# Performance work log

Hardware: AMD Instinct MI355X
Metric: run time of the kernel (lower is better)

## Reference

```python
import jax, jax.numpy as jnp
import numpy as np

B, T, I, H, NM = 128, 512, 2, 1024, 8
MS = H // NM  # module size = 128


def setup_inputs() -> dict:
    key = jax.random.key(0)
    ks = jax.random.split(key, 6)
    s = 1.0 / np.sqrt(H)
    return {
        "x": jax.random.normal(ks[0], (B, T + 1, I, 1), jnp.float32),
        "W_ih": jax.random.normal(ks[1], (H, I), jnp.float32) * s,
        "W_hh": jax.random.normal(ks[2], (H, H), jnp.float32) * s,
        "fc_w": jax.random.normal(ks[3], (I, H), jnp.float32) * s,
        "fc_b": jax.random.normal(ks[4], (I,), jnp.float32) * s,
        "enc_w": jax.random.normal(ks[5], (H, I), jnp.float32) * s,
    }


def reference(x, W_ih, W_hh, fc_w, fc_b, enc_w):
    # x: [B, T+1, I, 1] -> squeeze trailing dim
    xs = x[..., 0]                       # [B, T+1, I]
    h0 = xs[:, 0] @ enc_w.T              # start_encoder (no bias) -> [B, H]

    # Clockwork block structure: row-module i reads hidden cols >= i*MS.
    mod_idx = jnp.arange(H) // MS
    mask_hh = (mod_idx[None, :] >= mod_idx[:, None]).astype(W_hh.dtype)
    Whh_m = W_hh * mask_hh               # block upper-triangular recurrent weights
    periods = 2 ** jnp.arange(NM)        # module clock periods [1,2,4,...,128]

    def step(h, inp):
        x_t, t = inp                     # x_t: [B, I], t: scalar step index
        cand = jnp.tanh(x_t @ W_ih.T + h @ Whh_m.T)          # [B, H]
        active = jnp.repeat((t % periods) == 0, MS)          # [H] unit-level clock mask
        h_new = jnp.where(active[None, :], cand, h)          # inactive modules keep state
        return h_new, h_new @ fc_w.T + fc_b                  # fc output per step

    _, outs = jax.lax.scan(step, h0, (jnp.swapaxes(xs[:, 1:], 0, 1), jnp.arange(T)))
    return jnp.swapaxes(outs, 0, 1)      # [B, T, I]
```

## Files before the change

### kernel.cpp

```cpp
#include <hip/hip_runtime.h>
#include <hip/hip_fp16.h>
#include <math.h>

#define Bsz 128
#define Tsz 512
#define Hsz 1024
#define MS  128
#define NT  512


__global__ __launch_bounds__(256)
void retile_whh(const float* __restrict__ W, float* __restrict__ WB0,
                __half* __restrict__ WBr) {
    const int p = blockIdx.x;
    const int t = threadIdx.x;
    if (p == 0) {
        for (int idx = t; idx < MS*MS; idx += 256) {
            const int row = idx >> 7, j = idx & (MS-1);
            WB0[idx] = W[row * Hsz + j];
        }
        return;
    }
    int c = 0;
    while ((c+1)*(c+2)/2 <= p) ++c;
    const int r = p - c*(c+1)/2;
    __half* wb = WBr + (size_t)(p-1) * MS * MS;
    for (int idx = t; idx < MS*MS; idx += 256) {
        const int row = idx >> 7, j = idx & (MS-1);
        wb[idx] = __float2half(W[(size_t)(r*MS+row)*Hsz + c*MS + j]);
    }
}

__device__ __forceinline__ float fast_tanh(float x) {
    const float e = __expf(2.0f * x);
    return 1.0f - 2.0f * __builtin_amdgcn_rcpf(e + 1.0f);
}

template <int CTRL>
__device__ __forceinline__ float dpp_get(float v) {
    union { float f; int i; } u, o;
    u.f = v;
    o.i = __builtin_amdgcn_update_dpp(0, u.i, CTRL, 0xf, 0xf, true);
    return o.f;
}

union H4 { short4 s4; __half2 h2[2]; };

__global__ __launch_bounds__(NT)
void cwrnn_kernel(const float* __restrict__ x,
                  const float* __restrict__ W_ih,
                  const float* __restrict__ fc_w,
                  const float* __restrict__ fc_b,
                  const float* __restrict__ enc_w,
                  const float* __restrict__ WB0,
                  const __half* __restrict__ WBr,
                  float* __restrict__ out)
{
    __shared__ __half  WL[3][MS*136];
    __shared__ float   Sp2s[36][MS];
    __shared__ float   h_s[Hsz];
    __shared__ float   H0[2][MS];
    __shared__ float2  x_s[Tsz+1];
    __shared__ float2  wih_s[Hsz];
    __shared__ float2  fcw_s[Hsz];
    __shared__ float2  OpM0[2][8];
    __shared__ float2  OpHi[16];
    __shared__ float2  OpHiN[16];

    const int tid   = threadIdx.x;
    const int lane  = tid & 63;
    const int wave  = tid >> 6;
    const int b     = blockIdx.x;
    const int row00 = tid >> 2;
    const int jc    = tid & 3;

    const float2* xb = (const float2*)(x + (size_t)b*(Tsz+1)*2);
    float* outb = out + (size_t)b*Tsz*2;

    for (int i = tid; i < Tsz+1; i += NT) x_s[i] = xb[i];
    for (int i = tid; i < Hsz; i += NT) wih_s[i] = ((const float2*)W_ih)[i];
    for (int i = tid; i < Hsz; i += NT) fcw_s[i] = make_float2(fc_w[i], fc_w[Hsz+i]);
    for (int q = tid; q < 3*MS*16; q += NT) {
        const int pi = q / (MS*16), rem = q - pi*(MS*16);
        const int row = rem >> 4, k = rem & 15;
        const int p = (pi == 0) ? 2 : 3 + pi;
        *(int4*)(&WL[pi][row*136 + k*8]) =
            *(const int4*)(WBr + (size_t)(p-1)*MS*MS + row*MS + k*8);
    }
    if (tid < 16) { OpHi[tid] = make_float2(0.f,0.f); OpHiN[tid] = make_float2(0.f,0.f); }
    const float fb0 = fc_b[0], fb1 = fc_b[1];

    float4 w00[8];
    #pragma unroll
    for (int u = 0; u < 8; ++u) {
        const int uu = (u + 2*jc) & 7;
        w00[u] = *(const float4*)(WB0 + row00*MS + jc*32 + uu*4);
    }
    short4 w01[8], w02[8];
    #pragma unroll
    for (int u = 0; u < 8; ++u) {
        const int uu = (u + 2*jc) & 7;
        w01[u] = *(const short4*)(WBr + (size_t)0*MS*MS + row00*MS + jc*32 + uu*4);
        w02[u] = *(const short4*)(WBr + (size_t)2*MS*MS + row00*MS + jc*32 + uu*4);
    }

    {
        const float2 x0 = xb[0];
        for (int i = tid; i < Hsz; i += NT) {
            const float2 ew = ((const float2*)enc_w)[i];
            const float v = x0.x*ew.x + x0.y*ew.y;
            h_s[i] = v;
            if (i < MS) H0[0][i] = v;
        }
    }
    __syncthreads();

    float R1=0.f,R2=0.f,R3=0.f,R4=0.f,R5=0.f,R6=0.f,R7=0.f;

    auto load_hq = [&](int c, float4* hq) {
        #pragma unroll
        for (int u = 0; u < 8; ++u) {
            const int uu = (u + 2*jc) & 7;
            hq[u] = *(const float4*)(h_s + c*MS + jc*32 + uu*4);
        }
    };
    auto pair_acc = [&](const short4* w, const float4* hq) -> float {
        float a = 0.f;
        #pragma unroll
        for (int u = 0; u < 8; ++u) {
            H4 ww; ww.s4 = w[u];
            const float2 f01 = __half22float2(ww.h2[0]);
            const float2 f23 = __half22float2(ww.h2[1]);
            a += f01.x*hq[u].x + f01.y*hq[u].y + f23.x*hq[u].z + f23.y*hq[u].w;
        }
        return a;
    };
    auto wl_load = [&](int idx, short4* w) {
        const __half* base = WL[idx] + row00*136;
        #pragma unroll
        for (int u = 0; u < 8; ++u) {
            const int uu = (u + 2*jc) & 7;
            w[u] = *(const short4*)(base + jc*32 + uu*4);
        }
    };
    auto wg_load = [&](int p, short4* w) {
        const __half* base = WBr + (size_t)(p-1)*MS*MS + row00*MS;
        #pragma unroll
        for (int u = 0; u < 8; ++u) {
            const int uu = (u + 2*jc) & 7;
            w[u] = *(const short4*)(base + jc*32 + uu*4);
        }
    };

    auto do_cols = [&](int ashad) {
        float4 hq[8];
        short4 wA[8], wB[8];
        if (ashad >= 3) {
            load_hq(3, hq);
            wg_load(6, wA);
            int cc = 3, rr = 0;
            while (true) {
                int rn = rr + 1, cn = cc;
                if (rn > cn) { cn += 1; rn = 0; }
                const bool hn = (cn <= ashad);
                if (hn) wg_load(cn*(cn+1)/2 + rn, wB);
                float aa = pair_acc(wA, hq);
                if (rr == 0) {
                    switch (cc) {
                        case 3: R3 = aa; break;
                        case 4: R4 = aa; break;
                        case 5: R5 = aa; break;
                        case 6: R6 = aa; break;
                        default: R7 = aa; break;
                    }
                } else {
                    aa += dpp_get<0xB1>(aa); aa += dpp_get<0x4E>(aa);
                    if (jc == 0) Sp2s[cc*(cc+1)/2 + rr][row00] = aa;
                }
                if (!hn) break;
                if (cn != cc) load_hq(cn, hq);
                cc = cn; rr = rn;
                #pragma unroll
                for (int u = 0; u < 8; ++u) wA[u] = wB[u];
            }
        }
        load_hq(1, hq);
        R1 = pair_acc(w01, hq);
        wl_load(0, wA);
        { float aa = pair_acc(wA, hq);
          aa += dpp_get<0xB1>(aa); aa += dpp_get<0x4E>(aa);
          if (jc == 0) Sp2s[2][row00] = aa; }
        if (ashad >= 2) {
            load_hq(2, hq);
            R2 = pair_acc(w02, hq);
            wl_load(1, wA);
            { float aa = pair_acc(wA, hq);
              aa += dpp_get<0xB1>(aa); aa += dpp_get<0x4E>(aa);
              if (jc == 0) Sp2s[4][row00] = aa; }
            wl_load(2, wB);
            { float aa = pair_acc(wB, hq);
              aa += dpp_get<0xB1>(aa); aa += dpp_get<0x4E>(aa);
              if (jc == 0) Sp2s[5][row00] = aa; }
        }
    };

    do_cols(7);
    __syncthreads();

    for (int t = 0; t < Tsz; ++t) {
        const int A  = (t == 0) ? 7 : ((t & 1) ? 0 : min(__ffs(t)-1, 7));
        const int ap = (t & 1) ? ((t == 1) ? 7 : min(__ffs(t-1)-1, 7)) : 0;
        const float2 xt = x_s[t+1];

        if (ap >= 1) do_cols(ap);

        {
            const float* h0r = H0[t & 1];
            float a = 0.f;
            #pragma unroll
            for (int u = 0; u < 8; ++u) {
                const int uu = (u + 2*jc) & 7;
                const float4 hv = *(const float4*)(h0r + jc*32 + uu*4);
                a += w00[u].x*hv.x + w00[u].y*hv.y + w00[u].z*hv.z + w00[u].w*hv.w;
            }
            a += R1+R2+R3+R4+R5+R6+R7;
            a += dpp_get<0xB1>(a); a += dpp_get<0x4E>(a);
            const float2 wih0 = wih_s[row00];
            const float hv0 = fast_tanh(a + xt.x*wih0.x + xt.y*wih0.y);
            if (jc == 0) H0[(t+1)&1][row00] = hv0;
            const float2 fw0 = fcw_s[row00];
            float o0 = (jc == 0) ? hv0*fw0.x : 0.f;
            float o1 = (jc == 0) ? hv0*fw0.y : 0.f;
            o0 += dpp_get<0x111>(o0); o1 += dpp_get<0x111>(o1);
            o0 += dpp_get<0x112>(o0); o1 += dpp_get<0x112>(o1);
            o0 += dpp_get<0x114>(o0); o1 += dpp_get<0x114>(o1);
            o0 += dpp_get<0x118>(o0); o1 += dpp_get<0x118>(o1);
            o0 += dpp_get<0x142>(o0); o1 += dpp_get<0x142>(o1);
            o0 += dpp_get<0x143>(o0); o1 += dpp_get<0x143>(o1);
            if (lane == 63) OpM0[t&1][wave] = make_float2(o0, o1);
        }

        if (A >= 1) {
            const int nrows = (A+1)*MS;
            {
                const int g = MS + tid;
                if (g < nrows) {
                    const int r = g >> 7, il = g & (MS-1);
                    float sc[8];
                    #pragma unroll
                    for (int c = 1; c < 8; ++c)
                        sc[c] = Sp2s[c*(c+1)/2 + ((c < r) ? c : r)][il];
                    const float2 wih2 = wih_s[g];
                    float pre = xt.x*wih2.x + xt.y*wih2.y;
                    #pragma unroll
                    for (int c = 1; c < 8; ++c) pre += (c >= r) ? sc[c] : 0.f;
                    const float hv = fast_tanh(pre);
                    h_s[g] = hv;
                    const float2 fw = fcw_s[g];
                    float o0 = hv*fw.x, o1 = hv*fw.y;
                    o0 += dpp_get<0x111>(o0); o1 += dpp_get<0x111>(o1);
                    o0 += dpp_get<0x112>(o0); o1 += dpp_get<0x112>(o1);
                    o0 += dpp_get<0x114>(o0); o1 += dpp_get<0x114>(o1);
                    o0 += dpp_get<0x118>(o0); o1 += dpp_get<0x118>(o1);
                    o0 += dpp_get<0x142>(o0); o1 += dpp_get<0x142>(o1);
                    o0 += dpp_get<0x143>(o0); o1 += dpp_get<0x143>(o1);
                    if (lane == 63) OpHiN[2 + wave] = make_float2(o0, o1);
                }
            }
            {
                const int g = 5*MS + tid;
                if (g < nrows) {
                    const int r = g >> 7, il = g & (MS-1);
                    float sc[8];
                    #pragma unroll
                    for (int c = 1; c < 8; ++c)
                        sc[c] = Sp2s[c*(c+1)/2 + ((c < r) ? c : r)][il];
                    const float2 wih2 = wih_s[g];
                    float pre = xt.x*wih2.x + xt.y*wih2.y;
                    #pragma unroll
                    for (int c = 1; c < 8; ++c) pre += (c >= r) ? sc[c] : 0.f;
                    const float hv = fast_tanh(pre);
                    h_s[g] = hv;
                    const float2 fw = fcw_s[g];
                    float o0 = hv*fw.x, o1 = hv*fw.y;
                    o0 += dpp_get<0x111>(o0); o1 += dpp_get<0x111>(o1);
                    o0 += dpp_get<0x112>(o0); o1 += dpp_get<0x112>(o1);
                    o0 += dpp_get<0x114>(o0); o1 += dpp_get<0x114>(o1);
                    o0 += dpp_get<0x118>(o0); o1 += dpp_get<0x118>(o1);
                    o0 += dpp_get<0x142>(o0); o1 += dpp_get<0x142>(o1);
                    o0 += dpp_get<0x143>(o0); o1 += dpp_get<0x143>(o1);
                    if (lane == 63) OpHiN[10 + wave] = make_float2(o0, o1);
                }
            }
        }

        if (t > 0 && tid == 0) {
            const int tp = t - 1;
            if (ap >= 1) {
                for (int k = 2; k <= 2*ap+1; ++k) OpHi[k] = OpHiN[k];
            }
            float o0 = fb0, o1 = fb1;
            #pragma unroll
            for (int w = 0; w < 8; ++w) { o0 += OpM0[tp&1][w].x; o1 += OpM0[tp&1][w].y; }
            #pragma unroll
            for (int k = 2; k < 16; ++k) { o0 += OpHi[k].x; o1 += OpHi[k].y; }
            *(float2*)(outb + 2*tp) = make_float2(o0, o1);
        }

        __syncthreads();
    }

    if (tid == 0) {
        float o0 = fb0, o1 = fb1;
        #pragma unroll
        for (int w = 0; w < 8; ++w) { o0 += OpM0[1][w].x; o1 += OpM0[1][w].y; }
        #pragma unroll
        for (int k = 2; k < 16; ++k) { o0 += OpHi[k].x; o1 += OpHi[k].y; }
        *(float2*)(outb + 2*(Tsz-1)) = make_float2(o0, o1);
    }
}

extern "C" void kernel_launch(void* const* d_in, const int* in_sizes, int n_in,
                              void* d_out, int out_size, void* d_ws, size_t ws_size,
                              hipStream_t stream) {
    const float* x     = (const float*)d_in[0];
    const float* W_ih  = (const float*)d_in[1];
    const float* W_hh  = (const float*)d_in[2];
    const float* fc_w  = (const float*)d_in[3];
    const float* fc_b  = (const float*)d_in[4];
    const float* enc_w = (const float*)d_in[5];
    float* outp = (float*)d_out;
    float*  WB0 = (float*)d_ws;
    __half* WBr = (__half*)((char*)d_ws + 65536);

    retile_whh<<<36, 256, 0, stream>>>(W_hh, WB0, WBr);
    cwrnn_kernel<<<Bsz, NT, 0, stream>>>(x, W_ih, fc_w, fc_b, enc_w, WB0, WBr, outp);
}
```

Before: 974.7 us.

## Keep hot W_hh blocks fp32 in registers, drop LDS weight cache, use packed FMA

Blocks (0,1) and (1,1) of W_hh now stay in registers as fp32, read directly from W_hh, and the fp32 retile of block 0 is dropped. The LDS copy of three half-precision blocks is removed; those blocks are now streamed from global memory through the existing prefetch loop. Dot products use v_pk_fma_f32 with split accumulators. This trades register pressure and more global weight traffic for less LDS use and fewer FMA instructions, and it may shift the numerics slightly.

```diff
diff --git a/kernel.cpp b/kernel.cpp
--- a/kernel.cpp
+++ b/kernel.cpp
@@ -10,17 +10,9 @@
 
 
 __global__ __launch_bounds__(256)
-void retile_whh(const float* __restrict__ W, float* __restrict__ WB0,
-                __half* __restrict__ WBr) {
-    const int p = blockIdx.x;
+void retile_whh(const float* __restrict__ W, __half* __restrict__ WBr) {
+    const int p = blockIdx.x + 1;
     const int t = threadIdx.x;
-    if (p == 0) {
-        for (int idx = t; idx < MS*MS; idx += 256) {
-            const int row = idx >> 7, j = idx & (MS-1);
-            WB0[idx] = W[row * Hsz + j];
-        }
-        return;
-    }
     int c = 0;
     while ((c+1)*(c+2)/2 <= p) ++c;
     const int r = p - c*(c+1)/2;
@@ -44,7 +36,12 @@
     return o.f;
 }
 
+__device__ __forceinline__ void pk_fma(float2& acc, float2 a, float2 b) {
+    asm("v_pk_fma_f32 %0, %1, %2, %0" : "+v"(acc) : "v"(a), "v"(b));
+}
+
 union H4 { short4 s4; __half2 h2[2]; };
+union F4 { float4 v; float2 h[2]; };
 
 __global__ __launch_bounds__(NT)
 void cwrnn_kernel(const float* __restrict__ x,
@@ -52,11 +49,10 @@
                   const float* __restrict__ fc_w,
                   const float* __restrict__ fc_b,
                   const float* __restrict__ enc_w,
-                  const float* __restrict__ WB0,
+                  const float* __restrict__ Whh,
                   const __half* __restrict__ WBr,
                   float* __restrict__ out)
 {
-    __shared__ __half  WL[3][MS*136];
     __shared__ float   Sp2s[36][MS];
     __shared__ float   h_s[Hsz];
     __shared__ float   H0[2][MS];
@@ -80,27 +76,22 @@
     for (int i = tid; i < Tsz+1; i += NT) x_s[i] = xb[i];
     for (int i = tid; i < Hsz; i += NT) wih_s[i] = ((const float2*)W_ih)[i];
     for (int i = tid; i < Hsz; i += NT) fcw_s[i] = make_float2(fc_w[i], fc_w[Hsz+i]);
-    for (int q = tid; q < 3*MS*16; q += NT) {
-        const int pi = q / (MS*16), rem = q - pi*(MS*16);
-        const int row = rem >> 4, k = rem & 15;
-        const int p = (pi == 0) ? 2 : 3 + pi;
-        *(int4*)(&WL[pi][row*136 + k*8]) =
-            *(const int4*)(WBr + (size_t)(p-1)*MS*MS + row*MS + k*8);
-    }
     if (tid < 16) { OpHi[tid] = make_float2(0.f,0.f); OpHiN[tid] = make_float2(0.f,0.f); }
     const float fb0 = fc_b[0], fb1 = fc_b[1];
 
-    float4 w00[8];
+    F4 w00[8], w01[8], w11[8];
     #pragma unroll
     for (int u = 0; u < 8; ++u) {
         const int uu = (u + 2*jc) & 7;
-        w00[u] = *(const float4*)(WB0 + row00*MS + jc*32 + uu*4);
-    }
-    short4 w01[8], w02[8];
+        const int j  = jc*32 + uu*4;
+        w00[u].v = *(const float4*)(Whh + (size_t)row00*Hsz + j);
+        w01[u].v = *(const float4*)(Whh + (size_t)row00*Hsz + MS + j);
+        w11[u].v = *(const float4*)(Whh + (size_t)(MS + row00)*Hsz + MS + j);
+    }
+    short4 w02[8];
     #pragma unroll
     for (int u = 0; u < 8; ++u) {
         const int uu = (u + 2*jc) & 7;
-        w01[u] = *(const short4*)(WBr + (size_t)0*MS*MS + row00*MS + jc*32 + uu*4);
         w02[u] = *(const short4*)(WBr + (size_t)2*MS*MS + row00*MS + jc*32 + uu*4);
     }
 
@@ -117,54 +108,60 @@
 
     float R1=0.f,R2=0.f,R3=0.f,R4=0.f,R5=0.f,R6=0.f,R7=0.f;
 
-    auto load_hq = [&](int c, float4* hq) {
+    auto load_hq = [&](int c, F4* hq) {
         #pragma unroll
         for (int u = 0; u < 8; ++u) {
             const int uu = (u + 2*jc) & 7;
-            hq[u] = *(const float4*)(h_s + c*MS + jc*32 + uu*4);
-        }
-    };
-    auto pair_acc = [&](const short4* w, const float4* hq) -> float {
-        float a = 0.f;
+            hq[u].v = *(const float4*)(h_s + c*MS + jc*32 + uu*4);
+        }
+    };
+    auto pair_acc32 = [&](const F4* w, const F4* hq) -> float {
+        float2 a0 = {0.f,0.f}, a1 = {0.f,0.f};
+        #pragma unroll
+        for (int u = 0; u < 8; ++u) {
+            pk_fma(a0, w[u].h[0], hq[u].h[0]);
+            pk_fma(a1, w[u].h[1], hq[u].h[1]);
+        }
+        return (a0.x + a0.y) + (a1.x + a1.y);
+    };
+    auto pair_acc16 = [&](const short4* w, const F4* hq) -> float {
+        float2 a0 = {0.f,0.f}, a1 = {0.f,0.f};
         #pragma unroll
         for (int u = 0; u < 8; ++u) {
             H4 ww; ww.s4 = w[u];
-            const float2 f01 = __half22float2(ww.h2[0]);
-            const float2 f23 = __half22float2(ww.h2[1]);
-            a += f01.x*hq[u].x + f01.y*hq[u].y + f23.x*hq[u].z + f23.y*hq[u].w;
-        }
-        return a;
-    };
-    auto wl_load = [&](int idx, short4* w) {
-        const __half* base = WL[idx] + row00*136;
+            pk_fma(a0, __half22float2(ww.h2[0]), hq[u].h[0]);
+            pk_fma(a1, __half22float2(ww.h2[1]), hq[u].h[1]);
+        }
+        return (a0.x + a0.y) + (a1.x + a1.y);
+    };
+    auto wg_load = [&](int p, short4* w) {
+        const __half* base = WBr + (size_t)(p-1)*MS*MS + row00*MS;
         #pragma unroll
         for (int u = 0; u < 8; ++u) {
             const int uu = (u + 2*jc) & 7;
             w[u] = *(const short4*)(base + jc*32 + uu*4);
         }
     };
-    auto wg_load = [&](int p, short4* w) {
-        const __half* base = WBr + (size_t)(p-1)*MS*MS + row00*MS;
-        #pragma unroll
-        for (int u = 0; u < 8; ++u) {
-            const int uu = (u + 2*jc) & 7;
-            w[u] = *(const short4*)(base + jc*32 + uu*4);
-        }
-    };
 
     auto do_cols = [&](int ashad) {
-        float4 hq[8];
+        F4 hq[8];
         short4 wA[8], wB[8];
-        if (ashad >= 3) {
-            load_hq(3, hq);
-            wg_load(6, wA);
-            int cc = 3, rr = 0;
+        if (ashad >= 2) wg_load(4, wA);
+        load_hq(1, hq);
+        R1 = pair_acc32(w01, hq);
+        { float aa = pair_acc32(w11, hq);
+          aa += dpp_get<0xB1>(aa); aa += dpp_get<0x4E>(aa);
+          if (jc == 0) Sp2s[2][row00] = aa; }
+        if (ashad >= 2) {
+            load_hq(2, hq);
+            R2 = pair_acc16(w02, hq);
+            int cc = 2, rr = 1;
             while (true) {
                 int rn = rr + 1, cn = cc;
                 if (rn > cn) { cn += 1; rn = 0; }
                 const bool hn = (cn <= ashad);
                 if (hn) wg_load(cn*(cn+1)/2 + rn, wB);
-                float aa = pair_acc(wA, hq);
+                float aa = pair_acc16(wA, hq);
                 if (rr == 0) {
                     switch (cc) {
                         case 3: R3 = aa; break;
@@ -184,24 +181,6 @@
                 for (int u = 0; u < 8; ++u) wA[u] = wB[u];
             }
         }
-        load_hq(1, hq);
-        R1 = pair_acc(w01, hq);
-        wl_load(0, wA);
-        { float aa = pair_acc(wA, hq);
-          aa += dpp_get<0xB1>(aa); aa += dpp_get<0x4E>(aa);
-          if (jc == 0) Sp2s[2][row00] = aa; }
-        if (ashad >= 2) {
-            load_hq(2, hq);
-            R2 = pair_acc(w02, hq);
-            wl_load(1, wA);
-            { float aa = pair_acc(wA, hq);
-              aa += dpp_get<0xB1>(aa); aa += dpp_get<0x4E>(aa);
-              if (jc == 0) Sp2s[4][row00] = aa; }
-            wl_load(2, wB);
-            { float aa = pair_acc(wB, hq);
-              aa += dpp_get<0xB1>(aa); aa += dpp_get<0x4E>(aa);
-              if (jc == 0) Sp2s[5][row00] = aa; }
-        }
     };
 
     do_cols(7);
@@ -216,14 +195,16 @@
 
         {
             const float* h0r = H0[t & 1];
-            float a = 0.f;
+            float2 a0 = {0.f,0.f}, a1 = {0.f,0.f};
             #pragma unroll
             for (int u = 0; u < 8; ++u) {
                 const int uu = (u + 2*jc) & 7;
-                const float4 hv = *(const float4*)(h0r + jc*32 + uu*4);
-                a += w00[u].x*hv.x + w00[u].y*hv.y + w00[u].z*hv.z + w00[u].w*hv.w;
-            }
-            a += R1+R2+R3+R4+R5+R6+R7;
+                F4 hv; hv.v = *(const float4*)(h0r + jc*32 + uu*4);
+                pk_fma(a0, w00[u].h[0], hv.h[0]);
+                pk_fma(a1, w00[u].h[1], hv.h[1]);
+            }
+            float a = (a0.x + a0.y) + (a1.x + a1.y);
+            a += ((R1+R2)+(R3+R4)) + ((R5+R6)+R7);
             a += dpp_get<0xB1>(a); a += dpp_get<0x4E>(a);
             const float2 wih0 = wih_s[row00];
             const float hv0 = fast_tanh(a + xt.x*wih0.x + xt.y*wih0.y);
@@ -330,9 +311,8 @@
     const float* fc_b  = (const float*)d_in[4];
     const float* enc_w = (const float*)d_in[5];
     float* outp = (float*)d_out;
-    float*  WB0 = (float*)d_ws;
     __half* WBr = (__half*)((char*)d_ws + 65536);
 
-    retile_whh<<<36, 256, 0, stream>>>(W_hh, WB0, WBr);
-    cwrnn_kernel<<<Bsz, NT, 0, stream>>>(x, W_ih, fc_w, fc_b, enc_w, WB0, WBr, outp);
-}
+    retile_whh<<<35, 256, 0, stream>>>(W_hh, WBr);
+    cwrnn_kernel<<<Bsz, NT, 0, stream>>>(x, W_ih, fc_w, fc_b, enc_w, W_hh, WBr, outp);
+}
```

Measured after the change: 1.087 ms. +11.5%, slower.
